# Optimization experiments

Hardware: AMD Instinct MI355X
Metric: run time of the kernel (lower is better)

## Reference

```python
import jax, jax.numpy as jnp
import numpy as np

NUM_BLOCKS = 4
SPARSITY = 0.01
SCALE = 0.02


def _softshrink(x, lambd):
    return jnp.where(x > lambd, x - lambd, jnp.where(x < -lambd, x + lambd, 0.0))


def setup_inputs() -> dict:
    key = jax.random.key(0)
    k = jax.random.split(key, 5)
    B, N, C = 8, 4096, 768
    bs = C // NUM_BLOCKS
    return {
        "x": jax.random.normal(k[0], (B, N, C), dtype=jnp.float32),
        "complex_weight_1": jax.random.normal(k[1], (2, NUM_BLOCKS, bs, bs), dtype=jnp.float32) * SCALE,
        "complex_bias_1": jax.random.normal(k[2], (2, NUM_BLOCKS, bs), dtype=jnp.float32) * SCALE,
        "complex_weight_2": jax.random.normal(k[3], (2, NUM_BLOCKS, bs, bs), dtype=jnp.float32) * SCALE,
        "complex_bias_2": jax.random.normal(k[4], (2, NUM_BLOCKS, bs), dtype=jnp.float32) * SCALE,
    }


def reference(x, complex_weight_1, complex_bias_1, complex_weight_2, complex_bias_2):
    B, N, C = x.shape
    bs = C // NUM_BLOCKS
    xb = x.reshape(B, N, NUM_BLOCKS, bs)
    # FFT over (seq, block) axes, ortho norm -> complex64
    xf = jnp.fft.fft2(xb, axes=(1, 2), norm="ortho")

    mul = lambda t, w: jnp.einsum("snbd,bdk->snbk", t, w)

    w1, b1 = complex_weight_1, complex_bias_1
    w2, b2 = complex_weight_2, complex_bias_2

    xr, xi = xf.real, xf.imag
    r1 = jax.nn.relu(mul(xr, w1[0]) - mul(xi, w1[1]) + b1[0])
    i1 = jax.nn.relu(mul(xr, w1[1]) + mul(xi, w1[0]) + b1[1])
    r2 = mul(r1, w2[0]) - mul(i1, w2[1]) + b2[0]
    i2 = mul(r1, w2[1]) + mul(i1, w2[0]) + b2[1]

    r2 = _softshrink(r2, SPARSITY)
    i2 = _softshrink(i2, SPARSITY)

    z = jax.lax.complex(r2, i2)
    out = jnp.fft.ifft2(z, axes=(1, 2), norm="ortho").real.astype(jnp.float32)
    return out.reshape(B, N, C)
```

## Files before the change

### kernel.cpp

```cpp
#include <hip/hip_runtime.h>
#include <math.h>

#define N_SEQ   4096
#define C_TOT   768
#define NBLK    4
#define BS      192
#define B_BATCH 8
#define LAMBDA  0.01f
#define KTOT    384
#define APITCH  392
#define SW(x)   ((x) ^ (((x) >> 5) & 31))

typedef short    bf16x8  __attribute__((ext_vector_type(8)));
typedef short    short4v __attribute__((ext_vector_type(4)));
typedef float    f32x4   __attribute__((ext_vector_type(4)));
typedef unsigned short ushort_t;

__device__ __forceinline__ unsigned short f2bf(float f) {
  unsigned int u = __float_as_uint(f);
  u = (u + 0x7FFFu + ((u >> 16) & 1u)) >> 16;
  return (unsigned short)u;
}
__device__ __forceinline__ float b2f(unsigned short h) {
  return __uint_as_float(((unsigned int)h) << 16);
}

__device__ __forceinline__ void stockham_soa4(float* Ar, float* Ai,
                                              float* Br, float* Bi,
                                              int t, float sign) {
  float *sr = Ar, *si = Ai, *dr = Br, *di = Bi;
  float inv_p = 1.0f;
  int p = 1;
#pragma unroll
  for (int s = 0; s < 6; s++) {
#pragma unroll
    for (int m = 0; m < 2; m++) {
      int i = t + m * 512;
      int k = i & (p - 1);
      float a0r = sr[SW(i)],        a0i = si[SW(i)];
      float a1r = sr[SW(i + 1024)], a1i = si[SW(i + 1024)];
      float a2r = sr[SW(i + 2048)], a2i = si[SW(i + 2048)];
      float a3r = sr[SW(i + 3072)], a3i = si[SW(i + 3072)];
      float ang = sign * 1.5707963268f * inv_p * (float)k;
      float s1, c1;
      __sincosf(ang, &s1, &c1);
      float c2 = c1 * c1 - s1 * s1, s2 = 2.0f * c1 * s1;
      float c3 = c1 * c2 - s1 * s2, s3 = c1 * s2 + s1 * c2;
      float b1r = c1 * a1r - s1 * a1i, b1i = c1 * a1i + s1 * a1r;
      float b2r = c2 * a2r - s2 * a2i, b2i = c2 * a2i + s2 * a2r;
      float b3r = c3 * a3r - s3 * a3i, b3i = c3 * a3i + s3 * a3r;
      float t0r = a0r + b2r, t0i = a0i + b2i;
      float t1r = a0r - b2r, t1i = a0i - b2i;
      float t2r = b1r + b3r, t2i = b1i + b3i;
      float t3r = b1r - b3r, t3i = b1i - b3i;
      int j = ((i - k) << 2) + k;
      dr[SW(j)]         = t0r + t2r;        di[SW(j)]         = t0i + t2i;
      dr[SW(j + p)]     = t1r - sign * t3i; di[SW(j + p)]     = t1i + sign * t3r;
      dr[SW(j + 2 * p)] = t0r - t2r;        di[SW(j + 2 * p)] = t0i - t2i;
      dr[SW(j + 3 * p)] = t1r + sign * t3i; di[SW(j + 3 * p)] = t1i - sign * t3r;
    }
    __syncthreads();
    float* tp;
    tp = sr; sr = dr; dr = tp;
    tp = si; si = di; di = tp;
    p <<= 2;
    inv_p *= 0.25f;
  }
}

__global__ __launch_bounds__(256) void transpose_kernel(
    const float* __restrict__ src, float* __restrict__ dst, int R, int C) {
  __shared__ float tile[64][65];
  const int c0 = blockIdx.x * 64, r0 = blockIdx.y * 64, b = blockIdx.z;
  const int tid = threadIdx.x;
#pragma unroll
  for (int it = 0; it < 4; it++) {
    int g = it * 256 + tid;
    int r = g >> 4, q = g & 15;
    float4 v = *(const float4*)(src + ((size_t)b * R + r0 + r) * C + c0 + q * 4);
    tile[q * 4 + 0][r] = v.x;
    tile[q * 4 + 1][r] = v.y;
    tile[q * 4 + 2][r] = v.z;
    tile[q * 4 + 3][r] = v.w;
  }
  __syncthreads();
#pragma unroll
  for (int it = 0; it < 4; it++) {
    int g = it * 256 + tid;
    int c = g >> 4, w = g & 15;
    float4 v = make_float4(tile[c][w * 4 + 0], tile[c][w * 4 + 1],
                           tile[c][w * 4 + 2], tile[c][w * 4 + 3]);
    *(float4*)(dst + ((size_t)b * C + c0 + c) * R + r0 + w * 4) = v;
  }
}

__global__ __launch_bounds__(256) void prep_kernel(
    const float* __restrict__ w1, const float* __restrict__ w2,
    ushort_t* __restrict__ Bc) {
  int idx = blockIdx.x * 256 + threadIdx.x;
  int layer = idx / 589824; int r = idx - layer * 589824;
  int kb = r / 147456;      int r2 = r - kb * 147456;
  int jc = r2 / 6144;       int r3 = r2 - jc * 6144;
  int kc = r3 / 512;        int r4 = r3 - kc * 512;
  int lane = r4 >> 3;       int e = r4 & 7;
  int j = jc * 16 + (lane & 15);
  int k = kc * 32 + (lane >> 4) * 8 + e;
  const float* w = layer ? w2 : w1;
  float v;
  if (k < 192) {
    v = (j < 192) ? w[(kb * 192 + k) * 192 + j]
                  : w[((4 + kb) * 192 + k) * 192 + (j - 192)];
  } else {
    int k2 = k - 192;
    v = (j < 192) ? -w[((4 + kb) * 192 + k2) * 192 + j]
                  :  w[(kb * 192 + k2) * 192 + (j - 192)];
  }
  Bc[idx] = f2bf(v);
}

__global__ __launch_bounds__(512) void fft_fwd_kernel(
    const float* __restrict__ xT, ushort_t* __restrict__ Fr,
    ushort_t* __restrict__ Fi) {
  __shared__ float Ar[N_SEQ], Ai[N_SEQ], Br[N_SEQ], Bi[N_SEQ];
  const int q = blockIdx.x, b = blockIdx.y;
  const int c1 = 2 * q;
  const int t = threadIdx.x;
  const float* p1 = xT + ((size_t)b * C_TOT + c1) * N_SEQ;
  const float* p2 = p1 + N_SEQ;
#pragma unroll
  for (int m = 0; m < 8; m++) {
    int i = t + m * 512;
    Ar[SW(i)] = p1[i];
    Ai[SW(i)] = p2[i];
  }
  __syncthreads();
  stockham_soa4(Ar, Ai, Br, Bi, t, -1.0f);
  ushort_t* fr1 = Fr + ((size_t)b * C_TOT + c1) * N_SEQ;
  ushort_t* fi1 = Fi + ((size_t)b * C_TOT + c1) * N_SEQ;
#pragma unroll
  for (int m = 0; m < 8; m++) {
    int k = t + m * 512;
    int km = (N_SEQ - k) & (N_SEQ - 1);
    float a = Ar[SW(k)], bb = Ai[SW(k)], c = Ar[SW(km)], d = Ai[SW(km)];
    fr1[k]         = f2bf(0.5f * (a + c));
    fi1[k]         = f2bf(0.5f * (bb - d));
    fr1[N_SEQ + k] = f2bf(0.5f * (bb + d));
    fi1[N_SEQ + k] = f2bf(0.5f * (c - a));
  }
}

__global__ __launch_bounds__(256) void dft4t_kernel(
    const ushort_t* __restrict__ Fr, const ushort_t* __restrict__ Fi,
    ushort_t* __restrict__ Zb) {
  __shared__ ushort_t T[64 * APITCH];
  const int nt = blockIdx.x, kb = blockIdx.y, b = blockIdx.z;
  const int n0 = nt * 64;
  const int lane = threadIdx.x & 63, wave = threadIdx.x >> 6;
  const size_t S = (size_t)BS * N_SEQ;
  const float s = 0.0078125f;
  for (int dd = 0; dd < 48; dd++) {
    int d = wave * 48 + dd;
    size_t base = ((size_t)(b * C_TOT + d)) * N_SEQ + n0 + lane;
    float y0r = b2f(Fr[base]),         y0i = b2f(Fi[base]);
    float y1r = b2f(Fr[base + S]),     y1i = b2f(Fi[base + S]);
    float y2r = b2f(Fr[base + 2 * S]), y2i = b2f(Fi[base + 2 * S]);
    float y3r = b2f(Fr[base + 3 * S]), y3i = b2f(Fi[base + 3 * S]);
    float zr, zi;
    if (kb == 0)      { zr = y0r + y1r + y2r + y3r; zi = y0i + y1i + y2i + y3i; }
    else if (kb == 1) { zr = y0r + y1i - y2r - y3i; zi = y0i - y1r - y2i + y3r; }
    else if (kb == 2) { zr = y0r - y1r + y2r - y3r; zi = y0i - y1i + y2i - y3i; }
    else              { zr = y0r - y1i - y2r + y3i; zi = y0i + y1r - y2i - y3r; }
    T[lane * APITCH + d]       = f2bf(zr * s);
    T[lane * APITCH + 192 + d] = f2bf(zi * s);
  }
  __syncthreads();
  const size_t obase = ((size_t)((b * 4 + kb) * N_SEQ + n0)) * KTOT;
#pragma unroll
  for (int it = 0; it < 12; it++) {
    int g = it * 256 + threadIdx.x;
    int row = g / 48, c8 = g - row * 48;
    *(bf16x8*)(Zb + obase + (size_t)g * 8) =
        *(const bf16x8*)(&T[row * APITCH + c8 * 8]);
  }
}

__global__ __launch_bounds__(256, 2) void mlp_kernel(
    const ushort_t* __restrict__ Zb,
    const ushort_t* __restrict__ Bc,
    const float* __restrict__ b1g, const float* __restrict__ b2g,
    ushort_t* __restrict__ Or, ushort_t* __restrict__ Oi) {
  __shared__ ushort_t Abuf[64 * APITCH];
  const int nt = blockIdx.x, kb = blockIdx.y, b = blockIdx.z;
  const int n0 = nt * 64;
  const int tid = threadIdx.x;
  const int lane = tid & 63, wave = tid >> 6;
  const int fr = lane & 15, fg = lane >> 4;
  const int col0 = wave * 96;

  {
    const ushort_t* gsrc = Zb + ((size_t)((b * 4 + kb) * N_SEQ + n0)) * KTOT;
#pragma unroll
    for (int it = 0; it < 12; it++) {
      int g = it * 256 + tid;
      int row = g / 48, c8 = g - row * 48;
      *(bf16x8*)(&Abuf[row * APITCH + c8 * 8]) = *(const bf16x8*)(gsrc + (size_t)g * 8);
    }
  }
  __syncthreads();

  const ushort_t* B1 = Bc + (size_t)kb * 147456 + (size_t)wave * 36864 +
                       (size_t)lane * 8;
  const ushort_t* B2 = B1 + 589824;

  f32x4 acc[4][6];
  bf16x8 bf0[6], bf1[6], afr[4];

  auto loadB = [&](const ushort_t* Bb, int kc, bf16x8* dst) {
#pragma unroll
    for (int ct = 0; ct < 6; ct++)
      dst[ct] = *(const bf16x8*)(Bb + (size_t)kc * 512 + ct * 6144);
  };
  auto doK = [&](int kc, bf16x8* bw) {
#pragma unroll
    for (int rt = 0; rt < 4; rt++)
      afr[rt] = *(const bf16x8*)(&Abuf[(rt * 16 + fr) * APITCH + kc * 32 + fg * 8]);
#pragma unroll
    for (int rt = 0; rt < 4; rt++)
#pragma unroll
      for (int ct = 0; ct < 6; ct++)
        acc[rt][ct] = __builtin_amdgcn_mfma_f32_16x16x32_bf16(
            afr[rt], bw[ct], acc[rt][ct], 0, 0, 0);
  };

#pragma unroll
  for (int rt = 0; rt < 4; rt++)
#pragma unroll
    for (int ct = 0; ct < 6; ct++) acc[rt][ct] = 0.0f;
  loadB(B1, 0, bf0);
#pragma unroll
  for (int kc2 = 0; kc2 < 6; kc2++) {
    loadB(B1, 2 * kc2 + 1, bf1);
    doK(2 * kc2, bf0);
    if (kc2 < 5) loadB(B1, 2 * kc2 + 2, bf0);
    doK(2 * kc2 + 1, bf1);
  }

  __syncthreads();
#pragma unroll
  for (int ct = 0; ct < 6; ct++) {
    int j = col0 + ct * 16 + fr;
    float bias = (j < 192) ? b1g[kb * 192 + j] : b1g[768 + kb * 192 + (j - 192)];
#pragma unroll
    for (int rt = 0; rt < 4; rt++)
#pragma unroll
      for (int reg = 0; reg < 4; reg++) {
        float v = acc[rt][ct][reg] + bias;
        v = fmaxf(v, 0.0f);
        Abuf[(rt * 16 + fg * 4 + reg) * APITCH + j] = f2bf(v);
      }
  }
  __syncthreads();

#pragma unroll
  for (int rt = 0; rt < 4; rt++)
#pragma unroll
    for (int ct = 0; ct < 6; ct++) acc[rt][ct] = 0.0f;
  loadB(B2, 0, bf0);
#pragma unroll
  for (int kc2 = 0; kc2 < 6; kc2++) {
    loadB(B2, 2 * kc2 + 1, bf1);
    doK(2 * kc2, bf0);
    if (kc2 < 5) loadB(B2, 2 * kc2 + 2, bf0);
    doK(2 * kc2 + 1, bf1);
  }

#pragma unroll
  for (int ct = 0; ct < 6; ct++) {
    int j = col0 + ct * 16 + fr;
    float bias;
    ushort_t* plane;
    if (j < 192) {
      bias = b2g[kb * 192 + j];
      plane = Or + ((size_t)(b * C_TOT + kb * 192 + j)) * N_SEQ;
    } else {
      bias = b2g[768 + kb * 192 + (j - 192)];
      plane = Oi + ((size_t)(b * C_TOT + kb * 192 + (j - 192))) * N_SEQ;
    }
#pragma unroll
    for (int rt = 0; rt < 4; rt++) {
      short4v pk;
#pragma unroll
      for (int reg = 0; reg < 4; reg++) {
        float v = acc[rt][ct][reg] + bias;
        v = (v > LAMBDA) ? (v - LAMBDA) : ((v < -LAMBDA) ? (v + LAMBDA) : 0.0f);
        pk[reg] = (short)f2bf(v);
      }
      *(short4v*)(plane + n0 + rt * 16 + fg * 4) = pk;
    }
  }
}

__global__ __launch_bounds__(256) void dft4_inv_kernel(
    ushort_t* __restrict__ Or, ushort_t* __restrict__ Oi) {
  size_t tid8 = (size_t)blockIdx.x * 256 + threadIdx.x;
  int n8 = (int)(tid8 & 511);
  size_t rest = tid8 >> 9;
  int d = (int)(rest % BS);
  int b = (int)(rest / BS);
  size_t base = ((size_t)(b * C_TOT + d)) * N_SEQ + (size_t)n8 * 8;
  const size_t S = (size_t)BS * N_SEQ;
  bf16x8 z0r = *(const bf16x8*)(Or + base),         z0i = *(const bf16x8*)(Oi + base);
  bf16x8 z1r = *(const bf16x8*)(Or + base + S),     z1i = *(const bf16x8*)(Oi + base + S);
  bf16x8 z2r = *(const bf16x8*)(Or + base + 2 * S), z2i = *(const bf16x8*)(Oi + base + 2 * S);
  bf16x8 z3r = *(const bf16x8*)(Or + base + 3 * S), z3i = *(const bf16x8*)(Oi + base + 3 * S);
  bf16x8 o0r, o0i, o1r, o1i, o2r, o2i, o3r, o3i;
  const float s = 1.0f / 128.0f;
#pragma unroll
  for (int e = 0; e < 8; e++) {
    float a0r = b2f((unsigned short)z0r[e]), a0i = b2f((unsigned short)z0i[e]);
    float a1r = b2f((unsigned short)z1r[e]), a1i = b2f((unsigned short)z1i[e]);
    float a2r = b2f((unsigned short)z2r[e]), a2i = b2f((unsigned short)z2i[e]);
    float a3r = b2f((unsigned short)z3r[e]), a3i = b2f((unsigned short)z3i[e]);
    o0r[e] = (short)f2bf((a0r + a1r + a2r + a3r) * s);
    o0i[e] = (short)f2bf((a0i + a1i + a2i + a3i) * s);
    o1r[e] = (short)f2bf((a0r - a1i - a2r + a3i) * s);
    o1i[e] = (short)f2bf((a0i + a1r - a2i - a3r) * s);
    o2r[e] = (short)f2bf((a0r - a1r + a2r - a3r) * s);
    o2i[e] = (short)f2bf((a0i - a1i + a2i - a3i) * s);
    o3r[e] = (short)f2bf((a0r + a1i - a2r - a3i) * s);
    o3i[e] = (short)f2bf((a0i - a1r - a2i + a3r) * s);
  }
  *(bf16x8*)(Or + base)         = o0r; *(bf16x8*)(Oi + base)         = o0i;
  *(bf16x8*)(Or + base + S)     = o1r; *(bf16x8*)(Oi + base + S)     = o1i;
  *(bf16x8*)(Or + base + 2 * S) = o2r; *(bf16x8*)(Oi + base + 2 * S) = o2i;
  *(bf16x8*)(Or + base + 3 * S) = o3r; *(bf16x8*)(Oi + base + 3 * S) = o3i;
}

__global__ __launch_bounds__(512) void fft_inv_kernel(
    const ushort_t* __restrict__ Or, const ushort_t* __restrict__ Oi,
    float* __restrict__ yT) {
  __shared__ float Ar[N_SEQ], Ai[N_SEQ], Br[N_SEQ], Bi[N_SEQ];
  const int q = blockIdx.x, b = blockIdx.y;
  const int c1 = 2 * q;
  const int t = threadIdx.x;
  const ushort_t* zr1 = Or + ((size_t)b * C_TOT + c1) * N_SEQ;
  const ushort_t* zi1 = Oi + ((size_t)b * C_TOT + c1) * N_SEQ;
#pragma unroll
  for (int m = 0; m < 8; m++) {
    int i = t + m * 512;
    Ar[SW(i)] = b2f(zr1[i]);
    Ai[SW(i)] = b2f(zi1[i]);
    Br[SW(i)] = b2f(zr1[N_SEQ + i]);
    Bi[SW(i)] = b2f(zi1[N_SEQ + i]);
  }
  __syncthreads();
  float wr[8], wi[8];
#pragma unroll
  for (int m = 0; m < 8; m++) {
    int k = t + m * 512;
    int km = (N_SEQ - k) & (N_SEQ - 1);
    float zh1r = 0.5f * (Ar[SW(k)] + Ar[SW(km)]);
    float zh1i = 0.5f * (Ai[SW(k)] - Ai[SW(km)]);
    float zh2r = 0.5f * (Br[SW(k)] + Br[SW(km)]);
    float zh2i = 0.5f * (Bi[SW(k)] - Bi[SW(km)]);
    wr[m] = zh1r - zh2i;
    wi[m] = zh1i + zh2r;
  }
  __syncthreads();
#pragma unroll
  for (int m = 0; m < 8; m++) {
    int k = t + m * 512;
    Ar[SW(k)] = wr[m];
    Ai[SW(k)] = wi[m];
  }
  __syncthreads();
  stockham_soa4(Ar, Ai, Br, Bi, t, +1.0f);
  float* y1 = yT + ((size_t)b * C_TOT + c1) * N_SEQ;
#pragma unroll
  for (int m = 0; m < 8; m++) {
    int i = t + m * 512;
    y1[i]         = Ar[SW(i)];
    y1[N_SEQ + i] = Ai[SW(i)];
  }
}

extern "C" void kernel_launch(void* const* d_in, const int* in_sizes, int n_in,
                              void* d_out, int out_size, void* d_ws, size_t ws_size,
                              hipStream_t stream) {
  const float* x  = (const float*)d_in[0];
  const float* w1 = (const float*)d_in[1];
  const float* b1 = (const float*)d_in[2];
  const float* w2 = (const float*)d_in[3];
  const float* b2 = (const float*)d_in[4];
  float* out = (float*)d_out;

  const size_t P = (size_t)B_BATCH * C_TOT * N_SEQ;
  const size_t need = 8 * P + 2 * 589824 * sizeof(ushort_t);
  if (ws_size < need) return;
  char* base = (char*)d_ws;
  float*    xT = (float*)base;
  ushort_t* Zb = (ushort_t*)base;
  float*    yT = (float*)base;
  ushort_t* Fr = (ushort_t*)(base + 4 * P);
  ushort_t* Fi = (ushort_t*)(base + 6 * P);
  ushort_t* Bc = (ushort_t*)(base + 8 * P);

  hipLaunchKernelGGL(prep_kernel, dim3(4608), dim3(256), 0, stream, w1, w2, Bc);
  hipLaunchKernelGGL(transpose_kernel, dim3(C_TOT / 64, N_SEQ / 64, B_BATCH),
                     dim3(256), 0, stream, x, xT, N_SEQ, C_TOT);
  hipLaunchKernelGGL(fft_fwd_kernel, dim3(C_TOT / 2, B_BATCH), dim3(512), 0,
                     stream, xT, Fr, Fi);
  hipLaunchKernelGGL(dft4t_kernel, dim3(N_SEQ / 64, NBLK, B_BATCH), dim3(256),
                     0, stream, Fr, Fi, Zb);
  hipLaunchKernelGGL(mlp_kernel, dim3(N_SEQ / 64, NBLK, B_BATCH), dim3(256),
                     0, stream, Zb, Bc, b1, b2, Fr, Fi);
  hipLaunchKernelGGL(dft4_inv_kernel, dim3((B_BATCH * BS * N_SEQ / 8) / 256),
                     dim3(256), 0, stream, Fr, Fi);
  hipLaunchKernelGGL(fft_inv_kernel, dim3(C_TOT / 2, B_BATCH), dim3(512), 0,
                     stream, Fr, Fi, yT);
  hipLaunchKernelGGL(transpose_kernel, dim3(N_SEQ / 64, C_TOT / 64, B_BATCH),
                     dim3(256), 0, stream, yT, out, C_TOT, N_SEQ);
}
```

Baseline: 495.5 us.

## Fuse 4-point block DFTs into MLP and inverse FFT kernels, drop intermediate passes

After: 428.6 us. -13.5%, faster.

```diff
diff --git a/kernel.cpp b/kernel.cpp
--- a/kernel.cpp
+++ b/kernel.cpp
@@ -149,43 +149,8 @@
   }
 }
 
-__global__ __launch_bounds__(256) void dft4t_kernel(
+__global__ __launch_bounds__(256, 3) void mlp_kernel(
     const ushort_t* __restrict__ Fr, const ushort_t* __restrict__ Fi,
-    ushort_t* __restrict__ Zb) {
-  __shared__ ushort_t T[64 * APITCH];
-  const int nt = blockIdx.x, kb = blockIdx.y, b = blockIdx.z;
-  const int n0 = nt * 64;
-  const int lane = threadIdx.x & 63, wave = threadIdx.x >> 6;
-  const size_t S = (size_t)BS * N_SEQ;
-  const float s = 0.0078125f;
-  for (int dd = 0; dd < 48; dd++) {
-    int d = wave * 48 + dd;
-    size_t base = ((size_t)(b * C_TOT + d)) * N_SEQ + n0 + lane;
-    float y0r = b2f(Fr[base]),         y0i = b2f(Fi[base]);
-    float y1r = b2f(Fr[base + S]),     y1i = b2f(Fi[base + S]);
-    float y2r = b2f(Fr[base + 2 * S]), y2i = b2f(Fi[base + 2 * S]);
-    float y3r = b2f(Fr[base + 3 * S]), y3i = b2f(Fi[base + 3 * S]);
-    float zr, zi;
-    if (kb == 0)      { zr = y0r + y1r + y2r + y3r; zi = y0i + y1i + y2i + y3i; }
-    else if (kb == 1) { zr = y0r + y1i - y2r - y3i; zi = y0i - y1r - y2i + y3r; }
-    else if (kb == 2) { zr = y0r - y1r + y2r - y3r; zi = y0i - y1i + y2i - y3i; }
-    else              { zr = y0r - y1i - y2r + y3i; zi = y0i + y1r - y2i - y3r; }
-    T[lane * APITCH + d]       = f2bf(zr * s);
-    T[lane * APITCH + 192 + d] = f2bf(zi * s);
-  }
-  __syncthreads();
-  const size_t obase = ((size_t)((b * 4 + kb) * N_SEQ + n0)) * KTOT;
-#pragma unroll
-  for (int it = 0; it < 12; it++) {
-    int g = it * 256 + threadIdx.x;
-    int row = g / 48, c8 = g - row * 48;
-    *(bf16x8*)(Zb + obase + (size_t)g * 8) =
-        *(const bf16x8*)(&T[row * APITCH + c8 * 8]);
-  }
-}
-
-__global__ __launch_bounds__(256, 2) void mlp_kernel(
-    const ushort_t* __restrict__ Zb,
     const ushort_t* __restrict__ Bc,
     const float* __restrict__ b1g, const float* __restrict__ b2g,
     ushort_t* __restrict__ Or, ushort_t* __restrict__ Oi) {
@@ -198,12 +163,36 @@
   const int col0 = wave * 96;
 
   {
-    const ushort_t* gsrc = Zb + ((size_t)((b * 4 + kb) * N_SEQ + n0)) * KTOT;
-#pragma unroll
-    for (int it = 0; it < 12; it++) {
+    const size_t S = (size_t)BS * N_SEQ;
+    const float s = 0.0078125f;
+#pragma unroll
+    for (int it = 0; it < 6; it++) {
       int g = it * 256 + tid;
-      int row = g / 48, c8 = g - row * 48;
-      *(bf16x8*)(&Abuf[row * APITCH + c8 * 8]) = *(const bf16x8*)(gsrc + (size_t)g * 8);
+      int d = g >> 3, n8 = g & 7;
+      size_t bse = ((size_t)(b * C_TOT + d)) * N_SEQ + n0 + n8 * 8;
+      bf16x8 y0r = *(const bf16x8*)(Fr + bse);
+      bf16x8 y0i = *(const bf16x8*)(Fi + bse);
+      bf16x8 y1r = *(const bf16x8*)(Fr + bse + S);
+      bf16x8 y1i = *(const bf16x8*)(Fi + bse + S);
+      bf16x8 y2r = *(const bf16x8*)(Fr + bse + 2 * S);
+      bf16x8 y2i = *(const bf16x8*)(Fi + bse + 2 * S);
+      bf16x8 y3r = *(const bf16x8*)(Fr + bse + 3 * S);
+      bf16x8 y3i = *(const bf16x8*)(Fi + bse + 3 * S);
+#pragma unroll
+      for (int e = 0; e < 8; e++) {
+        float a0r = b2f((unsigned short)y0r[e]), a0i = b2f((unsigned short)y0i[e]);
+        float a1r = b2f((unsigned short)y1r[e]), a1i = b2f((unsigned short)y1i[e]);
+        float a2r = b2f((unsigned short)y2r[e]), a2i = b2f((unsigned short)y2i[e]);
+        float a3r = b2f((unsigned short)y3r[e]), a3i = b2f((unsigned short)y3i[e]);
+        float zr, zi;
+        if (kb == 0)      { zr = a0r + a1r + a2r + a3r; zi = a0i + a1i + a2i + a3i; }
+        else if (kb == 1) { zr = a0r + a1i - a2r - a3i; zi = a0i - a1r - a2i + a3r; }
+        else if (kb == 2) { zr = a0r - a1r + a2r - a3r; zi = a0i - a1i + a2i - a3i; }
+        else              { zr = a0r - a1i - a2r + a3i; zi = a0i + a1r - a2i - a3r; }
+        int n = n8 * 8 + e;
+        Abuf[n * APITCH + d]       = f2bf(zr * s);
+        Abuf[n * APITCH + 192 + d] = f2bf(zi * s);
+      }
     }
   }
   __syncthreads();
@@ -300,58 +289,50 @@
   }
 }
 
-__global__ __launch_bounds__(256) void dft4_inv_kernel(
-    ushort_t* __restrict__ Or, ushort_t* __restrict__ Oi) {
-  size_t tid8 = (size_t)blockIdx.x * 256 + threadIdx.x;
-  int n8 = (int)(tid8 & 511);
-  size_t rest = tid8 >> 9;
-  int d = (int)(rest % BS);
-  int b = (int)(rest / BS);
-  size_t base = ((size_t)(b * C_TOT + d)) * N_SEQ + (size_t)n8 * 8;
-  const size_t S = (size_t)BS * N_SEQ;
-  bf16x8 z0r = *(const bf16x8*)(Or + base),         z0i = *(const bf16x8*)(Oi + base);
-  bf16x8 z1r = *(const bf16x8*)(Or + base + S),     z1i = *(const bf16x8*)(Oi + base + S);
-  bf16x8 z2r = *(const bf16x8*)(Or + base + 2 * S), z2i = *(const bf16x8*)(Oi + base + 2 * S);
-  bf16x8 z3r = *(const bf16x8*)(Or + base + 3 * S), z3i = *(const bf16x8*)(Oi + base + 3 * S);
-  bf16x8 o0r, o0i, o1r, o1i, o2r, o2i, o3r, o3i;
-  const float s = 1.0f / 128.0f;
-#pragma unroll
-  for (int e = 0; e < 8; e++) {
-    float a0r = b2f((unsigned short)z0r[e]), a0i = b2f((unsigned short)z0i[e]);
-    float a1r = b2f((unsigned short)z1r[e]), a1i = b2f((unsigned short)z1i[e]);
-    float a2r = b2f((unsigned short)z2r[e]), a2i = b2f((unsigned short)z2i[e]);
-    float a3r = b2f((unsigned short)z3r[e]), a3i = b2f((unsigned short)z3i[e]);
-    o0r[e] = (short)f2bf((a0r + a1r + a2r + a3r) * s);
-    o0i[e] = (short)f2bf((a0i + a1i + a2i + a3i) * s);
-    o1r[e] = (short)f2bf((a0r - a1i - a2r + a3i) * s);
-    o1i[e] = (short)f2bf((a0i + a1r - a2i - a3r) * s);
-    o2r[e] = (short)f2bf((a0r - a1r + a2r - a3r) * s);
-    o2i[e] = (short)f2bf((a0i - a1i + a2i - a3i) * s);
-    o3r[e] = (short)f2bf((a0r + a1i - a2r - a3i) * s);
-    o3i[e] = (short)f2bf((a0i - a1r - a2i + a3r) * s);
-  }
-  *(bf16x8*)(Or + base)         = o0r; *(bf16x8*)(Oi + base)         = o0i;
-  *(bf16x8*)(Or + base + S)     = o1r; *(bf16x8*)(Oi + base + S)     = o1i;
-  *(bf16x8*)(Or + base + 2 * S) = o2r; *(bf16x8*)(Oi + base + 2 * S) = o2i;
-  *(bf16x8*)(Or + base + 3 * S) = o3r; *(bf16x8*)(Oi + base + 3 * S) = o3i;
-}
-
 __global__ __launch_bounds__(512) void fft_inv_kernel(
     const ushort_t* __restrict__ Or, const ushort_t* __restrict__ Oi,
     float* __restrict__ yT) {
   __shared__ float Ar[N_SEQ], Ai[N_SEQ], Br[N_SEQ], Bi[N_SEQ];
   const int q = blockIdx.x, b = blockIdx.y;
   const int c1 = 2 * q;
+  const int jb = c1 / 192;
+  const int d  = c1 - jb * 192;
   const int t = threadIdx.x;
-  const ushort_t* zr1 = Or + ((size_t)b * C_TOT + c1) * N_SEQ;
-  const ushort_t* zi1 = Oi + ((size_t)b * C_TOT + c1) * N_SEQ;
-#pragma unroll
-  for (int m = 0; m < 8; m++) {
-    int i = t + m * 512;
-    Ar[SW(i)] = b2f(zr1[i]);
-    Ai[SW(i)] = b2f(zi1[i]);
-    Br[SW(i)] = b2f(zr1[N_SEQ + i]);
-    Bi[SW(i)] = b2f(zi1[N_SEQ + i]);
+  const size_t S = (size_t)BS * N_SEQ;
+  const float s = 1.0f / 128.0f;
+  const size_t base0 = ((size_t)b * C_TOT + d) * N_SEQ;
+#pragma unroll
+  for (int m = 0; m < 2; m++) {
+    int i0 = m * 2048 + t * 4;
+#pragma unroll
+    for (int col = 0; col < 2; col++) {
+      size_t bse = base0 + (size_t)col * N_SEQ + i0;
+      short4v z0r = *(const short4v*)(Or + bse);
+      short4v z0i = *(const short4v*)(Oi + bse);
+      short4v z1r = *(const short4v*)(Or + bse + S);
+      short4v z1i = *(const short4v*)(Oi + bse + S);
+      short4v z2r = *(const short4v*)(Or + bse + 2 * S);
+      short4v z2i = *(const short4v*)(Oi + bse + 2 * S);
+      short4v z3r = *(const short4v*)(Or + bse + 3 * S);
+      short4v z3i = *(const short4v*)(Oi + bse + 3 * S);
+      float* Dr = col ? Br : Ar;
+      float* Di = col ? Bi : Ai;
+#pragma unroll
+      for (int e = 0; e < 4; e++) {
+        float a0r = b2f((unsigned short)z0r[e]), a0i = b2f((unsigned short)z0i[e]);
+        float a1r = b2f((unsigned short)z1r[e]), a1i = b2f((unsigned short)z1i[e]);
+        float a2r = b2f((unsigned short)z2r[e]), a2i = b2f((unsigned short)z2i[e]);
+        float a3r = b2f((unsigned short)z3r[e]), a3i = b2f((unsigned short)z3i[e]);
+        float orr, oii;
+        if (jb == 0)      { orr = a0r + a1r + a2r + a3r; oii = a0i + a1i + a2i + a3i; }
+        else if (jb == 1) { orr = a0r - a1i - a2r + a3i; oii = a0i + a1r - a2i - a3r; }
+        else if (jb == 2) { orr = a0r - a1r + a2r - a3r; oii = a0i - a1i + a2i - a3i; }
+        else              { orr = a0r + a1i - a2r - a3i; oii = a0i - a1r - a2i + a3r; }
+        int i = i0 + e;
+        Dr[SW(i)] = orr * s;
+        Di[SW(i)] = oii * s;
+      }
+    }
   }
   __syncthreads();
   float wr[8], wi[8];
@@ -398,11 +379,12 @@
   const size_t need = 8 * P + 2 * 589824 * sizeof(ushort_t);
   if (ws_size < need) return;
   char* base = (char*)d_ws;
-  float*    xT = (float*)base;
-  ushort_t* Zb = (ushort_t*)base;
+  ushort_t* Fr = (ushort_t*)base;
+  ushort_t* Fi = (ushort_t*)(base + 2 * P);
+  float*    xT = (float*)(base + 4 * P);
+  ushort_t* Or = (ushort_t*)(base + 4 * P);
+  ushort_t* Oi = (ushort_t*)(base + 6 * P);
   float*    yT = (float*)base;
-  ushort_t* Fr = (ushort_t*)(base + 4 * P);
-  ushort_t* Fi = (ushort_t*)(base + 6 * P);
   ushort_t* Bc = (ushort_t*)(base + 8 * P);
 
   hipLaunchKernelGGL(prep_kernel, dim3(4608), dim3(256), 0, stream, w1, w2, Bc);
@@ -410,14 +392,10 @@
                      dim3(256), 0, stream, x, xT, N_SEQ, C_TOT);
   hipLaunchKernelGGL(fft_fwd_kernel, dim3(C_TOT / 2, B_BATCH), dim3(512), 0,
                      stream, xT, Fr, Fi);
-  hipLaunchKernelGGL(dft4t_kernel, dim3(N_SEQ / 64, NBLK, B_BATCH), dim3(256),
-                     0, stream, Fr, Fi, Zb);
   hipLaunchKernelGGL(mlp_kernel, dim3(N_SEQ / 64, NBLK, B_BATCH), dim3(256),
-                     0, stream, Zb, Bc, b1, b2, Fr, Fi);
-  hipLaunchKernelGGL(dft4_inv_kernel, dim3((B_BATCH * BS * N_SEQ / 8) / 256),
-                     dim3(256), 0, stream, Fr, Fi);
+                     0, stream, Fr, Fi, Bc, b1, b2, Or, Oi);
   hipLaunchKernelGGL(fft_inv_kernel, dim3(C_TOT / 2, B_BATCH), dim3(512), 0,
-                     stream, Fr, Fi, yT);
+                     stream, Or, Oi, yT);
   hipLaunchKernelGGL(transpose_kernel, dim3(N_SEQ / 64, C_TOT / 64, B_BATCH),
                      dim3(256), 0, stream, yT, out, C_TOT, N_SEQ);
 }
```
